# Kernel tuning notes

Measured on AMD Instinct MI355X. Metric: run time of the kernel, lower is better.

The kernel has to match this reference:

```python
import jax, jax.numpy as jnp
import numpy as np

N_USERS, N_ITEMS = 100000, 50000
DIM_L, DIM_S, N_LAYERS = 128, 32, 4
DIM_C = 2 ** (N_LAYERS - 1) * DIM_L - 2 * DIM_S  # 960
BATCH = 131072
GLOBAL_AVG_MAIN = 3.5


def setup_inputs() -> dict:
    key = jax.random.key(0)
    ks = jax.random.split(key, 16)
    xav = lambda k, shp: jax.random.normal(k, shp, jnp.float32) * jnp.sqrt(2.0 / (shp[0] + shp[1]))
    inp = {
        "rows": jax.random.randint(ks[0], (BATCH,), 0, N_USERS, jnp.int64 if jax.config.jax_enable_x64 else jnp.int32),
        "cols": jax.random.randint(ks[1], (BATCH,), 0, N_ITEMS, jnp.int64 if jax.config.jax_enable_x64 else jnp.int32),
        "user_inter": xav(ks[2], (N_USERS, DIM_C)),
        "item_inter": xav(ks[3], (N_ITEMS, DIM_C)),
        "user_indep_x": xav(ks[4], (N_USERS, DIM_S)),
        "item_indep_x": xav(ks[5], (N_ITEMS, DIM_S)),
        "Wt": xav(ks[6], (DIM_C, DIM_C)),
        "bt": jnp.zeros((DIM_C,), jnp.float32),
        # f_x: widths 1024 -> 512 -> 256 -> 128 (Linear stored torch-style [out, in])
        "W1": xav(ks[7], (4 * DIM_L, 8 * DIM_L)),
        "b1": jnp.zeros((4 * DIM_L,), jnp.float32),
        "W2": xav(ks[8], (2 * DIM_L, 4 * DIM_L)),
        "b2": jnp.zeros((2 * DIM_L,), jnp.float32),
        "W3": xav(ks[9], (DIM_L, 2 * DIM_L)),
        "b3": jnp.zeros((DIM_L,), jnp.float32),
        "Wr": xav(ks[10], (1, DIM_L)),
        "br": jnp.zeros((1,), jnp.float32),
    }
    return inp


def reference(rows, cols, user_inter, item_inter, user_indep_x, item_indep_x,
              Wt, bt, W1, b1, W2, b2, W3, b3, Wr, br):
    # MAIN_MATRIX path, aux_type == TYPE_USER
    u_c = user_inter[rows]              # [B, dim_c]
    i_c = item_inter[cols]              # [B, dim_c]
    tu = u_c @ Wt.T + bt                # transfer_x(user_inter(rows))
    ti = i_c @ Wt.T + bt                # transfer_x(item_inter(cols))
    factor_inter = tu * ti              # [B, dim_c]
    factor = jnp.concatenate([user_indep_x[rows], item_indep_x[cols], factor_inter], axis=1)  # [B, 1024]
    factor = jnp.tanh(factor @ W1.T + b1)
    factor = jnp.tanh(factor @ W2.T + b2)
    factor = jnp.tanh(factor @ W3.T + b3)
    pred = factor @ Wr.T + br           # [B, 1]
    return pred + GLOBAL_AVG_MAIN
```

## Files before the change

### kernel.cpp

```cpp
#include <hip/hip_runtime.h>

typedef __attribute__((ext_vector_type(8))) short short8;
typedef __attribute__((ext_vector_type(4))) float f32x4;

__device__ inline unsigned short f2bf(float f) {
    union { float f; unsigned int u; } v; v.f = f;
    unsigned int u = v.u;
    unsigned int r = (u + 0x7FFFu + ((u >> 16) & 1u)) >> 16;
    return (unsigned short)r;
}
__device__ inline float bf2f(unsigned short u) {
    union { unsigned int u; float f; } v; v.u = ((unsigned int)u) << 16;
    return v.f;
}
__device__ inline void unpack2(unsigned int p, float& a, float& b) {
    union { unsigned int u; float f; } va, vb;
    va.u = p << 16;
    vb.u = p & 0xFFFF0000u;
    a = va.f; b = vb.f;
}
__device__ inline unsigned int pack2(float a, float b) {
    return (unsigned int)f2bf(a) | ((unsigned int)f2bf(b) << 16);
}
__device__ inline float fast_tanh(float x) {
    x = fminf(fmaxf(x, -15.f), 15.f);
    float e = __expf(2.f * x);
    return (e - 1.f) / (e + 1.f);
}
__device__ __forceinline__ void gld_lds16(const void* g, void* l) {
    __builtin_amdgcn_global_load_lds(
        (const __attribute__((address_space(1))) unsigned int*)g,
        (__attribute__((address_space(3))) unsigned int*)l, 16, 0, 0);
}

__global__ void convert_weights(const float* __restrict__ Wt, const float* __restrict__ W1,
                                const float* __restrict__ W2, const float* __restrict__ W3,
                                unsigned short* __restrict__ dst) {
    int idx = blockIdx.x * 256 + threadIdx.x;
    float v;
    if (idx < 921600) v = Wt[idx];
    else if (idx < 921600 + 524288) v = W1[idx - 921600];
    else if (idx < 921600 + 524288 + 131072) v = W2[idx - 921600 - 524288];
    else v = W3[idx - 921600 - 524288 - 131072];
    dst[idx] = f2bf(v);
}

__global__ void convert_f32_bf16(const float* __restrict__ src, unsigned short* __restrict__ dst, int n8) {
    int i = blockIdx.x * 256 + threadIdx.x;
    if (i >= n8) return;
    const float4* s = (const float4*)src + (size_t)i * 2;
    float4 a = s[0], b = s[1];
    uint4 o;
    o.x = pack2(a.x, a.y); o.y = pack2(a.z, a.w);
    o.z = pack2(b.x, b.y); o.w = pack2(b.z, b.w);
    ((uint4*)dst)[i] = o;
}

__global__ __launch_bounds__(256, 3) void transfer_gemm_fast(
    const unsigned short* __restrict__ A, int M,
    const unsigned short* __restrict__ Wt_bf, const float* __restrict__ bt,
    unsigned short* __restrict__ out) {
    __shared__ unsigned short lA[128 * 32];
    __shared__ unsigned short lB[192 * 32];

    const int nwg = gridDim.x * gridDim.y;
    const int orig = blockIdx.y * gridDim.x + blockIdx.x;
    const int qq = nwg >> 3, rr = nwg & 7;
    const int xcd = orig & 7, lo = orig >> 3;
    const int wgid = (xcd < rr ? xcd * (qq + 1) : rr * (qq + 1) + (xcd - rr) * qq) + lo;
    const int n0 = (wgid % gridDim.x) * 192;
    const int m0 = (wgid / gridDim.x) * 128;

    const int tid = threadIdx.x;
    const int wave = tid >> 6, lane = tid & 63;
    const int wm = wave & 1, wn = wave >> 1;
    const int q = lane >> 4, ra = lane & 15;

    const int lr = lane >> 2;
    const int lc = (lane & 3) * 8;
    const unsigned short* srcs[5];
    unsigned short* dsts[5];
#pragma unroll
    for (int j = 0; j < 5; j++) {
        int s = wave * 5 + j;
        if (s < 8) {
            int gr = m0 + s * 16 + lr; if (gr > M - 1) gr = M - 1;
            srcs[j] = A + (size_t)gr * 960 + lc;
            dsts[j] = &lA[s * 512];
        } else {
            int gr = n0 + (s - 8) * 16 + lr;
            srcs[j] = Wt_bf + (size_t)gr * 960 + lc;
            dsts[j] = &lB[(s - 8) * 512];
        }
    }

    f32x4 acc[4][6];
#pragma unroll
    for (int i = 0; i < 4; i++)
#pragma unroll
        for (int j = 0; j < 6; j++) acc[i][j] = (f32x4)0.f;

    for (int k0 = 0; k0 < 960; k0 += 32) {
#pragma unroll
        for (int j = 0; j < 5; j++) gld_lds16(srcs[j] + k0, dsts[j]);
        __syncthreads();
        short8 af[4];
#pragma unroll
        for (int mt = 0; mt < 4; mt++)
            af[mt] = *(const short8*)&lA[(wm * 64 + mt * 16 + ra) * 32 + q * 8];
#pragma unroll
        for (int nt = 0; nt < 6; nt++) {
            short8 bfr = *(const short8*)&lB[(wn * 96 + nt * 16 + ra) * 32 + q * 8];
#pragma unroll
            for (int mt = 0; mt < 4; mt++)
                acc[mt][nt] = __builtin_amdgcn_mfma_f32_16x16x32_bf16(af[mt], bfr, acc[mt][nt], 0, 0, 0);
        }
        __syncthreads();
    }
#pragma unroll
    for (int nt = 0; nt < 6; nt++) {
        int n = n0 + wn * 96 + nt * 16 + ra;
        float bias = bt[n];
#pragma unroll
        for (int mt = 0; mt < 4; mt++) {
#pragma unroll
            for (int i = 0; i < 4; i++) {
                int m = m0 + wm * 64 + mt * 16 + q * 4 + i;
                if (m < M) out[(size_t)m * 960 + n] = f2bf(acc[mt][nt][i] + bias);
            }
        }
    }
}

#define TG_LDA 40
#define TG_LDB 40
__global__ __launch_bounds__(512, 2) void transfer_gemm_slow(
    const float* __restrict__ A, int M,
    const unsigned short* __restrict__ Wt_bf, const float* __restrict__ bt,
    unsigned short* __restrict__ out) {
    __shared__ unsigned short lA[128 * TG_LDA];
    __shared__ unsigned short lB[192 * TG_LDB];
    const int n0 = blockIdx.x * 192;
    const int m0 = blockIdx.y * 128;
    const int tid = threadIdx.x;
    const int wave = tid >> 6, lane = tid & 63;
    const int wm = wave & 1, wn = wave >> 1;
    const int q = lane >> 4, ra = lane & 15;

    f32x4 acc[4][3];
#pragma unroll
    for (int i = 0; i < 4; i++)
#pragma unroll
        for (int j = 0; j < 3; j++) acc[i][j] = (f32x4)0.f;

    for (int k0 = 0; k0 < 960; k0 += 32) {
#pragma unroll
        for (int i = 0; i < 2; i++) {
            int idx = tid + i * 512;
            int row = idx >> 3, c4 = idx & 7;
            float4 f;
            if (m0 + row < M) f = *((const float4*)(A + (size_t)(m0 + row) * 960 + k0) + c4);
            else f = make_float4(0.f, 0.f, 0.f, 0.f);
            unsigned int p0 = pack2(f.x, f.y), p1 = pack2(f.z, f.w);
            *(uint2*)&lA[row * TG_LDA + c4 * 4] = make_uint2(p0, p1);
        }
#pragma unroll
        for (int i = 0; i < 3; i++) {
            int idx = tid + i * 512;
            int row = idx >> 3, c4 = idx & 7;
            uint2 d = *(const uint2*)(Wt_bf + (size_t)(n0 + row) * 960 + k0 + c4 * 4);
            *(uint2*)&lB[row * TG_LDB + c4 * 4] = d;
        }
        __syncthreads();
        short8 af[4];
#pragma unroll
        for (int mt = 0; mt < 4; mt++)
            af[mt] = *(const short8*)&lA[(wm * 64 + mt * 16 + ra) * TG_LDA + q * 8];
#pragma unroll
        for (int nt = 0; nt < 3; nt++) {
            short8 bfr = *(const short8*)&lB[(wn * 48 + nt * 16 + ra) * TG_LDB + q * 8];
#pragma unroll
            for (int mt = 0; mt < 4; mt++)
                acc[mt][nt] = __builtin_amdgcn_mfma_f32_16x16x32_bf16(af[mt], bfr, acc[mt][nt], 0, 0, 0);
        }
        __syncthreads();
    }
#pragma unroll
    for (int nt = 0; nt < 3; nt++) {
        int n = n0 + wn * 48 + nt * 16 + ra;
        float bias = bt[n];
#pragma unroll
        for (int mt = 0; mt < 4; mt++) {
#pragma unroll
            for (int i = 0; i < 4; i++) {
                int m = m0 + wm * 64 + mt * 16 + q * 4 + i;
                if (m < M) out[(size_t)m * 960 + n] = f2bf(acc[mt][nt][i] + bias);
            }
        }
    }
}

#define FC_LD 72
#define H1_LD 520
#define H2_LD 264
#define H3_LD 136
__global__ __launch_bounds__(256, 3) void fused_mlp(
    const int* __restrict__ rows, const int* __restrict__ cols,
    const float* __restrict__ ux, const float* __restrict__ ixp,
    const unsigned short* __restrict__ TU, const unsigned short* __restrict__ TI,
    const unsigned short* __restrict__ W1b, const float* __restrict__ b1,
    const unsigned short* __restrict__ W2b, const float* __restrict__ b2,
    const unsigned short* __restrict__ W3b, const float* __restrict__ b3,
    const float* __restrict__ Wr, const float* __restrict__ br,
    float* __restrict__ out) {
    __shared__ int s_row[32], s_col[32];
    __shared__ unsigned short fc2[2][32 * FC_LD];
    __shared__ unsigned short h1[32 * H1_LD];
    unsigned short* h2 = &fc2[0][0];
    unsigned short* h3 = &h1[0];

    const int tid = threadIdx.x;
    const int wave = tid >> 6, lane = tid & 63;
    const int q = lane >> 4, ra = lane & 15;
    const int r0 = blockIdx.x * 32;
    if (tid < 32) { s_row[tid] = rows[r0 + tid]; s_col[tid] = cols[r0 + tid]; }
    __syncthreads();

    const int srow = tid >> 3, g = tid & 7;
    const size_t tu_base = (size_t)s_row[srow] * 960;
    const size_t ti_base = (size_t)s_col[srow] * 960;

    f32x4 acc[2][8];
#pragma unroll
    for (int i = 0; i < 2; i++)
#pragma unroll
        for (int j = 0; j < 8; j++) acc[i][j] = (f32x4)0.f;

    uint4 val0;
    {
        const float* src = (g < 4) ? (ux + (size_t)s_row[srow] * 32 + g * 8)
                                   : (ixp + (size_t)s_col[srow] * 32 + (g - 4) * 8);
        float4 f0 = ((const float4*)src)[0];
        float4 f1 = ((const float4*)src)[1];
        val0.x = pack2(f0.x, f0.y); val0.y = pack2(f0.z, f0.w);
        val0.z = pack2(f1.x, f1.y); val0.w = pack2(f1.z, f1.w);
    }
    uint4 tu_r[2], ti_r[2];
    tu_r[1] = *(const uint4*)(TU + tu_base + g * 8);
    ti_r[1] = *(const uint4*)(TI + ti_base + g * 8);

#pragma unroll 2
    for (int kc = 0; kc < 16; kc++) {
        uint4 v;
        if (kc == 0) {
            v = val0;
        } else {
            uint4 tu8 = tu_r[kc & 1], ti8 = ti_r[kc & 1];
            float a0, a1, b0, b1f;
            unpack2(tu8.x, a0, a1); unpack2(ti8.x, b0, b1f); v.x = pack2(a0 * b0, a1 * b1f);
            unpack2(tu8.y, a0, a1); unpack2(ti8.y, b0, b1f); v.y = pack2(a0 * b0, a1 * b1f);
            unpack2(tu8.z, a0, a1); unpack2(ti8.z, b0, b1f); v.z = pack2(a0 * b0, a1 * b1f);
            unpack2(tu8.w, a0, a1); unpack2(ti8.w, b0, b1f); v.w = pack2(a0 * b0, a1 * b1f);
        }
        *(uint4*)&fc2[kc & 1][srow * FC_LD + g * 8] = v;
        __syncthreads();
        if (kc + 2 < 16) {
            int j0 = (kc + 1) * 64 + g * 8;
            tu_r[kc & 1] = *(const uint4*)(TU + tu_base + j0);
            ti_r[kc & 1] = *(const uint4*)(TI + ti_base + j0);
        }
#pragma unroll
        for (int ks = 0; ks < 2; ks++) {
            short8 a0 = *(const short8*)&fc2[kc & 1][(ra)*FC_LD + ks * 32 + q * 8];
            short8 a1 = *(const short8*)&fc2[kc & 1][(16 + ra) * FC_LD + ks * 32 + q * 8];
            int kg = kc * 64 + ks * 32;
#pragma unroll
            for (int nt = 0; nt < 8; nt++) {
                int n = wave * 128 + nt * 16 + ra;
                short8 b = *(const short8*)(W1b + (size_t)n * 1024 + kg + q * 8);
                acc[0][nt] = __builtin_amdgcn_mfma_f32_16x16x32_bf16(a0, b, acc[0][nt], 0, 0, 0);
                acc[1][nt] = __builtin_amdgcn_mfma_f32_16x16x32_bf16(a1, b, acc[1][nt], 0, 0, 0);
            }
        }
    }
    __syncthreads();
#pragma unroll
    for (int nt = 0; nt < 8; nt++) {
        int n = wave * 128 + nt * 16 + ra;
        float bias = b1[n];
#pragma unroll
        for (int mt = 0; mt < 2; mt++)
#pragma unroll
            for (int i = 0; i < 4; i++) {
                int m = mt * 16 + q * 4 + i;
                h1[m * H1_LD + n] = f2bf(fast_tanh(acc[mt][nt][i] + bias));
            }
    }
    __syncthreads();

    f32x4 acc2[2][4];
#pragma unroll
    for (int i = 0; i < 2; i++)
#pragma unroll
        for (int j = 0; j < 4; j++) acc2[i][j] = (f32x4)0.f;
    for (int k = 0; k < 512; k += 32) {
        short8 a0 = *(const short8*)&h1[(ra)*H1_LD + k + q * 8];
        short8 a1 = *(const short8*)&h1[(16 + ra) * H1_LD + k + q * 8];
#pragma unroll
        for (int nt = 0; nt < 4; nt++) {
            int n = wave * 64 + nt * 16 + ra;
            short8 b = *(const short8*)(W2b + (size_t)n * 512 + k + q * 8);
            acc2[0][nt] = __builtin_amdgcn_mfma_f32_16x16x32_bf16(a0, b, acc2[0][nt], 0, 0, 0);
            acc2[1][nt] = __builtin_amdgcn_mfma_f32_16x16x32_bf16(a1, b, acc2[1][nt], 0, 0, 0);
        }
    }
    __syncthreads();
#pragma unroll
    for (int nt = 0; nt < 4; nt++) {
        int n = wave * 64 + nt * 16 + ra;
        float bias = b2[n];
#pragma unroll
        for (int mt = 0; mt < 2; mt++)
#pragma unroll
            for (int i = 0; i < 4; i++) {
                int m = mt * 16 + q * 4 + i;
                h2[m * H2_LD + n] = f2bf(fast_tanh(acc2[mt][nt][i] + bias));
            }
    }
    __syncthreads();

    f32x4 acc3[2][2];
#pragma unroll
    for (int i = 0; i < 2; i++)
#pragma unroll
        for (int j = 0; j < 2; j++) acc3[i][j] = (f32x4)0.f;
    for (int k = 0; k < 256; k += 32) {
        short8 a0 = *(const short8*)&h2[(ra)*H2_LD + k + q * 8];
        short8 a1 = *(const short8*)&h2[(16 + ra) * H2_LD + k + q * 8];
#pragma unroll
        for (int nt = 0; nt < 2; nt++) {
            int n = wave * 32 + nt * 16 + ra;
            short8 b = *(const short8*)(W3b + (size_t)n * 256 + k + q * 8);
            acc3[0][nt] = __builtin_amdgcn_mfma_f32_16x16x32_bf16(a0, b, acc3[0][nt], 0, 0, 0);
            acc3[1][nt] = __builtin_amdgcn_mfma_f32_16x16x32_bf16(a1, b, acc3[1][nt], 0, 0, 0);
        }
    }
    __syncthreads();
#pragma unroll
    for (int nt = 0; nt < 2; nt++) {
        int n = wave * 32 + nt * 16 + ra;
        float bias = b3[n];
#pragma unroll
        for (int mt = 0; mt < 2; mt++)
#pragma unroll
            for (int i = 0; i < 4; i++) {
                int m = mt * 16 + q * 4 + i;
                h3[m * H3_LD + n] = f2bf(fast_tanh(acc3[mt][nt][i] + bias));
            }
    }
    __syncthreads();

    {
        int row = tid >> 3, seg = tid & 7;
        float s = 0.f;
#pragma unroll
        for (int i = 0; i < 16; i++) {
            int k = seg * 16 + i;
            s += bf2f(h3[row * H3_LD + k]) * Wr[k];
        }
        s += __shfl_xor(s, 1);
        s += __shfl_xor(s, 2);
        s += __shfl_xor(s, 4);
        if (seg == 0) out[r0 + row] = s + br[0] + 3.5f;
    }
}

extern "C" void kernel_launch(void* const* d_in, const int* in_sizes, int n_in,
                              void* d_out, int out_size, void* d_ws, size_t ws_size,
                              hipStream_t stream) {
    const int* rows = (const int*)d_in[0];
    const int* cols = (const int*)d_in[1];
    const float* user_inter = (const float*)d_in[2];
    const float* item_inter = (const float*)d_in[3];
    const float* ux = (const float*)d_in[4];
    const float* ixp = (const float*)d_in[5];
    const float* Wt = (const float*)d_in[6];
    const float* bt = (const float*)d_in[7];
    const float* W1 = (const float*)d_in[8];
    const float* b1 = (const float*)d_in[9];
    const float* W2 = (const float*)d_in[10];
    const float* b2 = (const float*)d_in[11];
    const float* W3 = (const float*)d_in[12];
    const float* b3 = (const float*)d_in[13];
    const float* Wr = (const float*)d_in[14];
    const float* br = (const float*)d_in[15];

    unsigned short* ws = (unsigned short*)d_ws;
    unsigned short* TU = ws;
    unsigned short* TI = ws + 96000000ull;

    const bool fast = (ws_size >= 483219456ull);

    if (fast) {
        unsigned short* Abf = ws + 144000000ull;
        unsigned short* Wt_bf = ws + 240000000ull;
        unsigned short* W1_bf = Wt_bf + 921600;
        unsigned short* W2_bf = W1_bf + 524288;
        unsigned short* W3_bf = W2_bf + 131072;

        convert_weights<<<6288, 256, 0, stream>>>(Wt, W1, W2, W3, Wt_bf);
        convert_f32_bf16<<<23438, 256, 0, stream>>>(item_inter, Abf, 6000000);
        transfer_gemm_fast<<<dim3(5, 391), 256, 0, stream>>>(Abf, 50000, Wt_bf, bt, TI);
        convert_f32_bf16<<<46875, 256, 0, stream>>>(user_inter, Abf, 12000000);
        transfer_gemm_fast<<<dim3(5, 782), 256, 0, stream>>>(Abf, 100000, Wt_bf, bt, TU);
        fused_mlp<<<4096, 256, 0, stream>>>(rows, cols, ux, ixp, TU, TI,
                                            W1_bf, b1, W2_bf, b2, W3_bf, b3, Wr, br,
                                            (float*)d_out);
    } else {
        unsigned short* Wt_bf = ws + 144000000ull;
        unsigned short* W1_bf = Wt_bf + 921600;
        unsigned short* W2_bf = W1_bf + 524288;
        unsigned short* W3_bf = W2_bf + 131072;

        convert_weights<<<6288, 256, 0, stream>>>(Wt, W1, W2, W3, Wt_bf);
        transfer_gemm_slow<<<dim3(5, 782), 512, 0, stream>>>(user_inter, 100000, Wt_bf, bt, TU);
        transfer_gemm_slow<<<dim3(5, 391), 512, 0, stream>>>(item_inter, 50000, Wt_bf, bt, TI);
        fused_mlp<<<4096, 256, 0, stream>>>(rows, cols, ux, ixp, TU, TI,
                                            W1_bf, b1, W2_bf, b2, W3_bf, b3, Wr, br,
                                            (float*)d_out);
    }
}
```

Measured before the change: 1.966 ms.

## Double fused MLP block to 512 threads, halving per-wave output columns

Runs the fused MLP kernel with 8 waves per block instead of 4. Each wave now computes half as many output columns in every layer, and each thread stages half as many gathered elements. The aim is fewer accumulator registers per thread and more waves to hide the gather and weight-load latency. In exchange, every block does twice as many barriers' worth of waiting, and the A-fragment LDS reads are duplicated across more waves.

```diff
diff --git a/kernel.cpp b/kernel.cpp
--- a/kernel.cpp
+++ b/kernel.cpp
@@ -204,7 +204,7 @@
 #define H1_LD 520
 #define H2_LD 264
 #define H3_LD 136
-__global__ __launch_bounds__(256, 3) void fused_mlp(
+__global__ __launch_bounds__(512, 6) void fused_mlp(
     const int* __restrict__ rows, const int* __restrict__ cols,
     const float* __restrict__ ux, const float* __restrict__ ixp,
     const unsigned short* __restrict__ TU, const unsigned short* __restrict__ TI,
@@ -226,48 +226,44 @@
     if (tid < 32) { s_row[tid] = rows[r0 + tid]; s_col[tid] = cols[r0 + tid]; }
     __syncthreads();
 
-    const int srow = tid >> 3, g = tid & 7;
+    const int srow = tid >> 4, g = tid & 15;
     const size_t tu_base = (size_t)s_row[srow] * 960;
     const size_t ti_base = (size_t)s_col[srow] * 960;
 
-    f32x4 acc[2][8];
+    f32x4 acc[2][4];
 #pragma unroll
     for (int i = 0; i < 2; i++)
 #pragma unroll
-        for (int j = 0; j < 8; j++) acc[i][j] = (f32x4)0.f;
-
-    uint4 val0;
+        for (int j = 0; j < 4; j++) acc[i][j] = (f32x4)0.f;
+
+    uint2 val0;
     {
-        const float* src = (g < 4) ? (ux + (size_t)s_row[srow] * 32 + g * 8)
-                                   : (ixp + (size_t)s_col[srow] * 32 + (g - 4) * 8);
+        const float* src = (g < 8) ? (ux + (size_t)s_row[srow] * 32 + g * 4)
+                                   : (ixp + (size_t)s_col[srow] * 32 + (g - 8) * 4);
         float4 f0 = ((const float4*)src)[0];
-        float4 f1 = ((const float4*)src)[1];
         val0.x = pack2(f0.x, f0.y); val0.y = pack2(f0.z, f0.w);
-        val0.z = pack2(f1.x, f1.y); val0.w = pack2(f1.z, f1.w);
-    }
-    uint4 tu_r[2], ti_r[2];
-    tu_r[1] = *(const uint4*)(TU + tu_base + g * 8);
-    ti_r[1] = *(const uint4*)(TI + ti_base + g * 8);
+    }
+    uint2 tu_r[2], ti_r[2];
+    tu_r[1] = *(const uint2*)(TU + tu_base + g * 4);
+    ti_r[1] = *(const uint2*)(TI + ti_base + g * 4);
 
 #pragma unroll 2
     for (int kc = 0; kc < 16; kc++) {
-        uint4 v;
+        uint2 v;
         if (kc == 0) {
             v = val0;
         } else {
-            uint4 tu8 = tu_r[kc & 1], ti8 = ti_r[kc & 1];
+            uint2 tu8 = tu_r[kc & 1], ti8 = ti_r[kc & 1];
             float a0, a1, b0, b1f;
             unpack2(tu8.x, a0, a1); unpack2(ti8.x, b0, b1f); v.x = pack2(a0 * b0, a1 * b1f);
             unpack2(tu8.y, a0, a1); unpack2(ti8.y, b0, b1f); v.y = pack2(a0 * b0, a1 * b1f);
-            unpack2(tu8.z, a0, a1); unpack2(ti8.z, b0, b1f); v.z = pack2(a0 * b0, a1 * b1f);
-            unpack2(tu8.w, a0, a1); unpack2(ti8.w, b0, b1f); v.w = pack2(a0 * b0, a1 * b1f);
-        }
-        *(uint4*)&fc2[kc & 1][srow * FC_LD + g * 8] = v;
+        }
+        *(uint2*)&fc2[kc & 1][srow * FC_LD + g * 4] = v;
         __syncthreads();
         if (kc + 2 < 16) {
-            int j0 = (kc + 1) * 64 + g * 8;
-            tu_r[kc & 1] = *(const uint4*)(TU + tu_base + j0);
-            ti_r[kc & 1] = *(const uint4*)(TI + ti_base + j0);
+            int j0 = (kc + 1) * 64 + g * 4;
+            tu_r[kc & 1] = *(const uint2*)(TU + tu_base + j0);
+            ti_r[kc & 1] = *(const uint2*)(TI + ti_base + j0);
         }
 #pragma unroll
         for (int ks = 0; ks < 2; ks++) {
@@ -275,8 +271,8 @@
             short8 a1 = *(const short8*)&fc2[kc & 1][(16 + ra) * FC_LD + ks * 32 + q * 8];
             int kg = kc * 64 + ks * 32;
 #pragma unroll
-            for (int nt = 0; nt < 8; nt++) {
-                int n = wave * 128 + nt * 16 + ra;
+            for (int nt = 0; nt < 4; nt++) {
+                int n = wave * 64 + nt * 16 + ra;
                 short8 b = *(const short8*)(W1b + (size_t)n * 1024 + kg + q * 8);
                 acc[0][nt] = __builtin_amdgcn_mfma_f32_16x16x32_bf16(a0, b, acc[0][nt], 0, 0, 0);
                 acc[1][nt] = __builtin_amdgcn_mfma_f32_16x16x32_bf16(a1, b, acc[1][nt], 0, 0, 0);
@@ -285,8 +281,8 @@
     }
     __syncthreads();
 #pragma unroll
-    for (int nt = 0; nt < 8; nt++) {
-        int n = wave * 128 + nt * 16 + ra;
+    for (int nt = 0; nt < 4; nt++) {
+        int n = wave * 64 + nt * 16 + ra;
         float bias = b1[n];
 #pragma unroll
         for (int mt = 0; mt < 2; mt++)
@@ -298,17 +294,17 @@
     }
     __syncthreads();
 
-    f32x4 acc2[2][4];
+    f32x4 acc2[2][2];
 #pragma unroll
     for (int i = 0; i < 2; i++)
 #pragma unroll
-        for (int j = 0; j < 4; j++) acc2[i][j] = (f32x4)0.f;
+        for (int j = 0; j < 2; j++) acc2[i][j] = (f32x4)0.f;
     for (int k = 0; k < 512; k += 32) {
         short8 a0 = *(const short8*)&h1[(ra)*H1_LD + k + q * 8];
         short8 a1 = *(const short8*)&h1[(16 + ra) * H1_LD + k + q * 8];
 #pragma unroll
-        for (int nt = 0; nt < 4; nt++) {
-            int n = wave * 64 + nt * 16 + ra;
+        for (int nt = 0; nt < 2; nt++) {
+            int n = wave * 32 + nt * 16 + ra;
             short8 b = *(const short8*)(W2b + (size_t)n * 512 + k + q * 8);
             acc2[0][nt] = __builtin_amdgcn_mfma_f32_16x16x32_bf16(a0, b, acc2[0][nt], 0, 0, 0);
             acc2[1][nt] = __builtin_amdgcn_mfma_f32_16x16x32_bf16(a1, b, acc2[1][nt], 0, 0, 0);
@@ -316,8 +312,8 @@
     }
     __syncthreads();
 #pragma unroll
-    for (int nt = 0; nt < 4; nt++) {
-        int n = wave * 64 + nt * 16 + ra;
+    for (int nt = 0; nt < 2; nt++) {
+        int n = wave * 32 + nt * 16 + ra;
         float bias = b2[n];
 #pragma unroll
         for (int mt = 0; mt < 2; mt++)
@@ -329,48 +325,42 @@
     }
     __syncthreads();
 
-    f32x4 acc3[2][2];
-#pragma unroll
-    for (int i = 0; i < 2; i++)
-#pragma unroll
-        for (int j = 0; j < 2; j++) acc3[i][j] = (f32x4)0.f;
+    f32x4 acc3[2];
+    acc3[0] = (f32x4)0.f; acc3[1] = (f32x4)0.f;
     for (int k = 0; k < 256; k += 32) {
         short8 a0 = *(const short8*)&h2[(ra)*H2_LD + k + q * 8];
         short8 a1 = *(const short8*)&h2[(16 + ra) * H2_LD + k + q * 8];
-#pragma unroll
-        for (int nt = 0; nt < 2; nt++) {
-            int n = wave * 32 + nt * 16 + ra;
-            short8 b = *(const short8*)(W3b + (size_t)n * 256 + k + q * 8);
-            acc3[0][nt] = __builtin_amdgcn_mfma_f32_16x16x32_bf16(a0, b, acc3[0][nt], 0, 0, 0);
-            acc3[1][nt] = __builtin_amdgcn_mfma_f32_16x16x32_bf16(a1, b, acc3[1][nt], 0, 0, 0);
-        }
-    }
-    __syncthreads();
-#pragma unroll
-    for (int nt = 0; nt < 2; nt++) {
-        int n = wave * 32 + nt * 16 + ra;
+        int n = wave * 16 + ra;
+        short8 b = *(const short8*)(W3b + (size_t)n * 256 + k + q * 8);
+        acc3[0] = __builtin_amdgcn_mfma_f32_16x16x32_bf16(a0, b, acc3[0], 0, 0, 0);
+        acc3[1] = __builtin_amdgcn_mfma_f32_16x16x32_bf16(a1, b, acc3[1], 0, 0, 0);
+    }
+    __syncthreads();
+    {
+        int n = wave * 16 + ra;
         float bias = b3[n];
 #pragma unroll
         for (int mt = 0; mt < 2; mt++)
 #pragma unroll
             for (int i = 0; i < 4; i++) {
                 int m = mt * 16 + q * 4 + i;
-                h3[m * H3_LD + n] = f2bf(fast_tanh(acc3[mt][nt][i] + bias));
+                h3[m * H3_LD + n] = f2bf(fast_tanh(acc3[mt][i] + bias));
             }
     }
     __syncthreads();
 
     {
-        int row = tid >> 3, seg = tid & 7;
+        int row = tid >> 4, seg = tid & 15;
         float s = 0.f;
 #pragma unroll
-        for (int i = 0; i < 16; i++) {
-            int k = seg * 16 + i;
+        for (int i = 0; i < 8; i++) {
+            int k = seg * 8 + i;
             s += bf2f(h3[row * H3_LD + k]) * Wr[k];
         }
         s += __shfl_xor(s, 1);
         s += __shfl_xor(s, 2);
         s += __shfl_xor(s, 4);
+        s += __shfl_xor(s, 8);
         if (seg == 0) out[r0 + row] = s + br[0] + 3.5f;
     }
 }
@@ -413,7 +403,7 @@
         transfer_gemm_fast<<<dim3(5, 391), 256, 0, stream>>>(Abf, 50000, Wt_bf, bt, TI);
         convert_f32_bf16<<<46875, 256, 0, stream>>>(user_inter, Abf, 12000000);
         transfer_gemm_fast<<<dim3(5, 782), 256, 0, stream>>>(Abf, 100000, Wt_bf, bt, TU);
-        fused_mlp<<<4096, 256, 0, stream>>>(rows, cols, ux, ixp, TU, TI,
+        fused_mlp<<<4096, 512, 0, stream>>>(rows, cols, ux, ixp, TU, TI,
                                             W1_bf, b1, W2_bf, b2, W3_bf, b3, Wr, br,
                                             (float*)d_out);
     } else {
@@ -425,7 +415,7 @@
         convert_weights<<<6288, 256, 0, stream>>>(Wt, W1, W2, W3, Wt_bf);
         transfer_gemm_slow<<<dim3(5, 782), 512, 0, stream>>>(user_inter, 100000, Wt_bf, bt, TU);
         transfer_gemm_slow<<<dim3(5, 391), 512, 0, stream>>>(item_inter, 50000, Wt_bf, bt, TI);
-        fused_mlp<<<4096, 256, 0, stream>>>(rows, cols, ux, ixp, TU, TI,
+        fused_mlp<<<4096, 512, 0, stream>>>(rows, cols, ux, ixp, TU, TI,
                                             W1_bf, b1, W2_bf, b2, W3_bf, b3, Wr, br,
                                             (float*)d_out);
     }
```

Measured after the change: 1.992 ms. Within noise of the previous version (+1.3%).
